# Kernel tuning notes

Hardware: AMD Instinct MI355X
Metric: run time of the kernel (lower is better)

Reference implementation:

```python
import jax, jax.numpy as jnp
import numpy as np

D_MODEL = 512
NUM_HEADS = 8
D_K = D_MODEL // NUM_HEADS


def _linear(x, w, b):
    # torch nn.Linear: y = x @ w.T + b, w: [out, in]
    return jnp.einsum('bsd,ed->bse', x, w) + b


def _attn_proj(x, w1, b1, w2, b2):
    return jax.nn.silu(_linear(x, w1, b1)) * _linear(x, w2, b2)


def setup_inputs() -> dict:
    key = jax.random.key(0)
    ks = jax.random.split(key, 20)
    B, S, D = 4, 8192, D_MODEL
    scale = 1.0 / np.sqrt(D)
    inp = {
        'query': jax.random.normal(ks[0], (B, S, D), jnp.float32),
        'key': jax.random.normal(ks[1], (B, S, D), jnp.float32),
        'value': jax.random.normal(ks[2], (B, S, D), jnp.float32),
    }
    names = ['q_w1', 'q_w2', 'k_w1', 'k_w2', 'v_w1', 'v_w2', 'out_w']
    for i, n in enumerate(names):
        inp[n] = jax.random.normal(ks[3 + i], (D, D), jnp.float32) * scale
    bnames = ['q_b1', 'q_b2', 'k_b1', 'k_b2', 'v_b1', 'v_b2', 'out_b']
    for i, n in enumerate(bnames):
        inp[n] = jax.random.normal(ks[10 + i], (D,), jnp.float32) * 0.01
    return inp


def reference(query, key, value,
              q_w1, q_w2, k_w1, k_w2, v_w1, v_w2, out_w,
              q_b1, q_b2, k_b1, k_b2, v_b1, v_b2, out_b):
    B = query.shape[0]
    eps = 1e-6
    # projections -> [B, H, S, d_k]
    def split_heads(x):
        return x.reshape(B, -1, NUM_HEADS, D_K).transpose(0, 2, 1, 3)
    q = split_heads(_attn_proj(query, q_w1, q_b1, q_w2, q_b2))
    k = split_heads(_attn_proj(key, k_w1, k_b1, k_w2, k_b2))
    v = split_heads(_attn_proj(value, v_w1, v_b1, v_w2, v_b2))

    phi_q = jax.nn.elu(q) + 1.0
    phi_k = jax.nn.elu(k) + 1.0
    # key_value: [B, H, d_k, d_k]
    key_value = jnp.einsum('bhsd,bhse->bhde', phi_k, v)
    key_sum = phi_k.sum(axis=-2)                       # [B, H, d_k]
    qk_sum = jnp.einsum('bhsd,bhd->bhs', phi_q, key_sum)
    numerator = jnp.einsum('bhsd,bhde->bhse', phi_q, key_value)
    attn = numerator / (qk_sum[..., None] + eps)       # [B, H, S, d_k]

    x = attn.transpose(0, 2, 1, 3).reshape(B, -1, NUM_HEADS * D_K)
    return _linear(x, out_w, out_b)
```

## Files before the change

### kernel.cpp

```cpp
#include <hip/hip_runtime.h>
#include <stdint.h>


#define DMODEL 512
#define NHEAD 8
#define BATCH 4
#define SEQ 8192
#define BSROWS (BATCH * SEQ)
#define NSPLIT 16
#define CHUNK (SEQ / NSPLIT)

typedef __attribute__((ext_vector_type(8))) short short8;
typedef __attribute__((ext_vector_type(4))) short short4v;
typedef __attribute__((ext_vector_type(4))) float f32x4;
typedef __attribute__((ext_vector_type(4))) unsigned short ushort4v;

__device__ __forceinline__ unsigned short f2bf(float f) {
  union { float f; uint32_t u; } v; v.f = f;
  uint32_t u = v.u;
  u += 0x7fffu + ((u >> 16) & 1u);
  return (unsigned short)(u >> 16);
}
__device__ __forceinline__ float bf2f(unsigned short h) {
  union { float f; uint32_t u; } v; v.u = ((uint32_t)h) << 16; return v.f;
}
__device__ __forceinline__ f32x4 zero4() {
  f32x4 z; z[0] = 0.f; z[1] = 0.f; z[2] = 0.f; z[3] = 0.f; return z;
}
__device__ __forceinline__ void gload_lds16(const unsigned short* g, unsigned short* l) {
  __builtin_amdgcn_global_load_lds((const __attribute__((address_space(1))) void*)g,
                                   (__attribute__((address_space(3))) void*)l, 16, 0, 0);
}

struct WPtrs { const float* w[7]; };

__global__ void convert_weights_kernel(WPtrs wp, unsigned short* __restrict__ wbf) {
  int gid = blockIdx.x * 256 + threadIdx.x;
  int which = gid >> 16;
  int rem = gid & 65535;
  float4 v = ((const float4*)wp.w[which])[rem];
  ushort4v o;
  o[0] = f2bf(v.x); o[1] = f2bf(v.y); o[2] = f2bf(v.z); o[3] = f2bf(v.w);
  *(ushort4v*)(wbf + (size_t)which * 262144 + (size_t)rem * 4) = o;
}

__global__ void convert_x_kernel(const float* __restrict__ q, const float* __restrict__ k,
                                 const float* __restrict__ v, unsigned short* __restrict__ xbf) {
  size_t t = (size_t)blockIdx.x * 256 + threadIdx.x;
  int which = (int)(t >> 21);
  size_t rem = t & 2097151;
  const float* src = which == 0 ? q : (which == 1 ? k : v);
  const float4* s4 = (const float4*)src + rem * 2;
  float4 a = s4[0], b = s4[1];
  short8 o;
  o[0] = (short)f2bf(a.x); o[1] = (short)f2bf(a.y);
  o[2] = (short)f2bf(a.z); o[3] = (short)f2bf(a.w);
  o[4] = (short)f2bf(b.x); o[5] = (short)f2bf(b.y);
  o[6] = (short)f2bf(b.z); o[7] = (short)f2bf(b.w);
  *(short8*)(xbf + ((size_t)which << 24) + rem * 8) = o;
}

struct ProjArgs {
  const float* b1[3];
  const float* b2[3];
  unsigned short* out[3];
};

__global__ __launch_bounds__(256, 2) void proj_kernel(ProjArgs pa,
                                                      const unsigned short* __restrict__ wbf,
                                                      const unsigned short* __restrict__ xbf) {
  const int which = blockIdx.y;
  const unsigned short* __restrict__ x = xbf + ((size_t)which << 24);
  const unsigned short* __restrict__ w1 = wbf + (size_t)which * 524288;
  const unsigned short* __restrict__ w2 = w1 + 262144;
  const float* __restrict__ b1p = pa.b1[which];
  const float* __restrict__ b2p = pa.b2[which];
  unsigned short* __restrict__ outp = pa.out[which];
  const bool PHI = (which < 2);

  const int mt = blockIdx.x >> 2, nt = blockIdx.x & 3;
  const int m0 = mt * 128, n0 = nt * 128;
  const int tid = threadIdx.x;
  const int wave = tid >> 6, lane = tid & 63;
  const int lrow = lane & 15, quad = lane >> 4;
  const int m_off = (wave & 1) * 64, n_off = (wave >> 1) * 64;

  __shared__ unsigned short sA[128 * 64];
  __shared__ unsigned short sB1[128 * 64];
  __shared__ unsigned short sB2[128 * 64];

  const int srow_l = lane >> 3;
  const int kq_l = (lane & 7) ^ srow_l;
  const int swz = lrow & 7;

  f32x4 acc1[4][4], acc2[4][4];
#pragma unroll
  for (int i = 0; i < 4; i++)
#pragma unroll
    for (int j = 0; j < 4; j++) { acc1[i][j] = zero4(); acc2[i][j] = zero4(); }

  for (int k0 = 0; k0 < 512; k0 += 64) {
    __syncthreads();
#pragma unroll
    for (int i = 0; i < 4; i++) {
      int ig = wave * 4 + i;
      size_t roff = (size_t)(ig * 8 + srow_l) * 512 + k0 + kq_l * 8;
      gload_lds16(x + (size_t)m0 * 512 + roff, sA + ig * 512);
      gload_lds16(w1 + (size_t)n0 * 512 + roff, sB1 + ig * 512);
      gload_lds16(w2 + (size_t)n0 * 512 + roff, sB2 + ig * 512);
    }
    __syncthreads();
#pragma unroll
    for (int kk = 0; kk < 64; kk += 32) {
      const int e8 = (kk >> 3) + quad;
      short8 af[4], b1f[4], b2f[4];
#pragma unroll
      for (int mi = 0; mi < 4; mi++)
        af[mi] = *(const short8*)(sA + (m_off + mi * 16 + lrow) * 64 + (((e8 ^ swz) << 3)));
#pragma unroll
      for (int ni = 0; ni < 4; ni++) {
        int rr = n_off + ni * 16 + lrow;
        b1f[ni] = *(const short8*)(sB1 + rr * 64 + (((e8 ^ swz) << 3)));
        b2f[ni] = *(const short8*)(sB2 + rr * 64 + (((e8 ^ swz) << 3)));
      }
#pragma unroll
      for (int ni = 0; ni < 4; ni++)
#pragma unroll
        for (int mi = 0; mi < 4; mi++) {
          acc1[mi][ni] = __builtin_amdgcn_mfma_f32_16x16x32_bf16(af[mi], b1f[ni], acc1[mi][ni], 0, 0, 0);
          acc2[mi][ni] = __builtin_amdgcn_mfma_f32_16x16x32_bf16(af[mi], b2f[ni], acc2[mi][ni], 0, 0, 0);
        }
    }
  }

  if (which == 0) {
#pragma unroll
    for (int ni = 0; ni < 4; ni++) {
      int n = n0 + n_off + ni * 16 + lrow;
      float bb1 = b1p[n], bb2 = b2p[n];
#pragma unroll
      for (int mi = 0; mi < 4; mi++)
#pragma unroll
        for (int r = 0; r < 4; r++) {
          int m = m0 + m_off + mi * 16 + quad * 4 + r;
          float v1 = acc1[mi][ni][r] + bb1;
          float v2 = acc2[mi][ni][r] + bb2;
          float y = v1 * (1.f / (1.f + __expf(-v1))) * v2;
          y = (y > 0.f) ? (y + 1.f) : __expf(y);
          outp[(size_t)m * 512 + n] = f2bf(y);
        }
    }
  } else {
    const int bI = m0 >> 13;
    const int sb = (m0 & 8191) + m_off + quad * 4;
#pragma unroll
    for (int ni = 0; ni < 4; ni++) {
      int n = n0 + n_off + ni * 16 + lrow;
      float bb1 = b1p[n], bb2 = b2p[n];
      int h = n >> 6, d = n & 63;
      unsigned short* dst0 = outp + (((size_t)bI * 8 + h) * 64 + d) * 8192 + sb;
#pragma unroll
      for (int mi = 0; mi < 4; mi++) {
        short4v o;
#pragma unroll
        for (int r = 0; r < 4; r++) {
          float v1 = acc1[mi][ni][r] + bb1;
          float v2 = acc2[mi][ni][r] + bb2;
          float y = v1 * (1.f / (1.f + __expf(-v1))) * v2;
          if (PHI) y = (y > 0.f) ? (y + 1.f) : __expf(y);
          o[r] = (short)f2bf(y);
        }
        *(short4v*)(dst0 + mi * 16) = o;
      }
    }
  }
}

__global__ __launch_bounds__(256) void kv_kernel(const unsigned short* __restrict__ kT,
                                                 const unsigned short* __restrict__ vT,
                                                 float* __restrict__ kvt_part,
                                                 float* __restrict__ ksum_part) {
  const int chunk = blockIdx.x & (NSPLIT - 1);
  const int bh = blockIdx.x >> 4;
  const int tid = threadIdx.x;
  const int wave = tid >> 6, lane = tid & 63;
  const int lrow = lane & 15, quad = lane >> 4;

  __shared__ float ls_acc[4096];
  __shared__ float ls_ksum[64];
  if (tid < 64) ls_ksum[tid] = 0.f;
#pragma unroll
  for (int i = 0; i < 16; i++) ls_acc[tid + 256 * i] = 0.f;

  const unsigned short* vrow = vT + (size_t)bh * 64 * 8192;
  const unsigned short* krow = kT + (size_t)bh * 64 * 8192;
  const int s_w = chunk * CHUNK + wave * 128;

  short8 ones;
#pragma unroll
  for (int j = 0; j < 8; j++) ones[j] = (short)0x3F80;

  f32x4 acc[4][4], aks[4];
#pragma unroll
  for (int i = 0; i < 4; i++) {
    aks[i] = zero4();
#pragma unroll
    for (int j = 0; j < 4; j++) acc[i][j] = zero4();
  }

  for (int it = 0; it < 4; it++) {
    const int s0 = s_w + it * 32 + quad * 8;
    short8 af[4], bfr[4];
#pragma unroll
    for (int mi = 0; mi < 4; mi++)
      af[mi] = *(const short8*)(vrow + (size_t)(mi * 16 + lrow) * 8192 + s0);
#pragma unroll
    for (int ni = 0; ni < 4; ni++)
      bfr[ni] = *(const short8*)(krow + (size_t)(ni * 16 + lrow) * 8192 + s0);
#pragma unroll
    for (int ni = 0; ni < 4; ni++) {
      aks[ni] = __builtin_amdgcn_mfma_f32_16x16x32_bf16(ones, bfr[ni], aks[ni], 0, 0, 0);
#pragma unroll
      for (int mi = 0; mi < 4; mi++)
        acc[mi][ni] = __builtin_amdgcn_mfma_f32_16x16x32_bf16(af[mi], bfr[ni], acc[mi][ni], 0, 0, 0);
    }
  }

  __syncthreads();
#pragma unroll
  for (int mi = 0; mi < 4; mi++)
#pragma unroll
    for (int ni = 0; ni < 4; ni++)
#pragma unroll
      for (int r = 0; r < 4; r++)
        atomicAdd(&ls_acc[(mi * 16 + quad * 4 + r) * 64 + ni * 16 + lrow], acc[mi][ni][r]);
  if (quad == 0) {
#pragma unroll
    for (int ni = 0; ni < 4; ni++) atomicAdd(&ls_ksum[ni * 16 + lrow], aks[ni][0]);
  }
  __syncthreads();

  float* op = kvt_part + ((size_t)chunk * 32 + bh) * 4096;
#pragma unroll
  for (int i = 0; i < 16; i++) op[tid + 256 * i] = ls_acc[tid + 256 * i];
  if (tid < 64) ksum_part[((size_t)chunk * 32 + bh) * 64 + tid] = ls_ksum[tid];
}

__global__ void kv_reduce_kernel(const float* __restrict__ kvt_part,
                                 const float* __restrict__ ksum_part,
                                 unsigned short* __restrict__ kvT,
                                 unsigned short* __restrict__ ksum_bf) {
  const int bh = blockIdx.x >> 2, seg = blockIdx.x & 3;
  const int idx = seg * 1024 + threadIdx.x * 4;
  float4 s = make_float4(0.f, 0.f, 0.f, 0.f);
#pragma unroll
  for (int c = 0; c < NSPLIT; c++) {
    float4 v = *(const float4*)&kvt_part[((size_t)c * 32 + bh) * 4096 + idx];
    s.x += v.x; s.y += v.y; s.z += v.z; s.w += v.w;
  }
  ushort4v o;
  o[0] = f2bf(s.x); o[1] = f2bf(s.y); o[2] = f2bf(s.z); o[3] = f2bf(s.w);
  *(ushort4v*)(kvT + (size_t)bh * 4096 + idx) = o;
  if (seg == 0 && threadIdx.x < 64) {
    float t = 0.f;
#pragma unroll
    for (int c = 0; c < NSPLIT; c++) t += ksum_part[((size_t)c * 32 + bh) * 64 + threadIdx.x];
    ksum_bf[bh * 64 + threadIdx.x] = f2bf(t);
  }
}

__global__ __launch_bounds__(256) void attn_kernel(const unsigned short* __restrict__ phiQ,
                                                   const unsigned short* __restrict__ kvT,
                                                   const unsigned short* __restrict__ ksum_bf,
                                                   unsigned short* __restrict__ xattn) {
  const int bh = blockIdx.x & 31;
  const int st = blockIdx.x >> 5;
  const int b = bh >> 3, h = bh & 7;
  const int tid = threadIdx.x;
  const int wave = tid >> 6, lane = tid & 63;
  const int lrow = lane & 15, quad = lane >> 4;
  const size_t rowbase = (size_t)b * SEQ + st * 128 + wave * 32;

  f32x4 acc[2][4], aqs[2];
#pragma unroll
  for (int i = 0; i < 2; i++) {
    aqs[i] = zero4();
#pragma unroll
    for (int j = 0; j < 4; j++) acc[i][j] = zero4();
  }

#pragma unroll
  for (int kk = 0; kk < 64; kk += 32) {
    short8 ks = *(const short8*)(ksum_bf + bh * 64 + kk + quad * 8);
    short8 af[2];
#pragma unroll
    for (int mi = 0; mi < 2; mi++)
      af[mi] = *(const short8*)(phiQ + (rowbase + mi * 16 + lrow) * 512 + h * 64 + kk + quad * 8);
#pragma unroll
    for (int mi = 0; mi < 2; mi++)
      aqs[mi] = __builtin_amdgcn_mfma_f32_16x16x32_bf16(af[mi], ks, aqs[mi], 0, 0, 0);
#pragma unroll
    for (int ni = 0; ni < 4; ni++) {
      short8 bfr = *(const short8*)(kvT + (size_t)bh * 4096 + (ni * 16 + lrow) * 64 + kk + quad * 8);
#pragma unroll
      for (int mi = 0; mi < 2; mi++)
        acc[mi][ni] = __builtin_amdgcn_mfma_f32_16x16x32_bf16(af[mi], bfr, acc[mi][ni], 0, 0, 0);
    }
  }
#pragma unroll
  for (int mi = 0; mi < 2; mi++) {
#pragma unroll
    for (int r = 0; r < 4; r++) {
      float inv = 1.f / (aqs[mi][r] + 1e-6f);
      size_t m = rowbase + mi * 16 + quad * 4 + r;
#pragma unroll
      for (int ni = 0; ni < 4; ni++)
        xattn[m * 512 + h * 64 + ni * 16 + lrow] = f2bf(acc[mi][ni][r] * inv);
    }
  }
}

__global__ __launch_bounds__(256, 2) void out_gemm_kernel(const unsigned short* __restrict__ xattn,
                                                          const unsigned short* __restrict__ wo,
                                                          const float* __restrict__ ob,
                                                          float* __restrict__ out) {
  const int mt = blockIdx.x >> 2, nt = blockIdx.x & 3;
  const int m0 = mt * 128, n0 = nt * 128;
  const int tid = threadIdx.x;
  const int wave = tid >> 6, lane = tid & 63;
  const int lrow = lane & 15, quad = lane >> 4;
  const int m_off = (wave & 1) * 64, n_off = (wave >> 1) * 64;

  __shared__ unsigned short sA[128 * 64];
  __shared__ unsigned short sB[128 * 64];

  const int srow_l = lane >> 3;
  const int kq_l = (lane & 7) ^ srow_l;
  const int swz = lrow & 7;

  f32x4 acc[4][4];
#pragma unroll
  for (int i = 0; i < 4; i++)
#pragma unroll
    for (int j = 0; j < 4; j++) acc[i][j] = zero4();

  for (int k0 = 0; k0 < 512; k0 += 64) {
    __syncthreads();
#pragma unroll
    for (int i = 0; i < 4; i++) {
      int ig = wave * 4 + i;
      size_t roff = (size_t)(ig * 8 + srow_l) * 512 + k0 + kq_l * 8;
      gload_lds16(xattn + (size_t)m0 * 512 + roff, sA + ig * 512);
      gload_lds16(wo + (size_t)n0 * 512 + roff, sB + ig * 512);
    }
    __syncthreads();
#pragma unroll
    for (int kk = 0; kk < 64; kk += 32) {
      const int e8 = (kk >> 3) + quad;
      short8 af[4], bfr[4];
#pragma unroll
      for (int mi = 0; mi < 4; mi++)
        af[mi] = *(const short8*)(sA + (m_off + mi * 16 + lrow) * 64 + (((e8 ^ swz) << 3)));
#pragma unroll
      for (int ni = 0; ni < 4; ni++)
        bfr[ni] = *(const short8*)(sB + (n_off + ni * 16 + lrow) * 64 + (((e8 ^ swz) << 3)));
#pragma unroll
      for (int ni = 0; ni < 4; ni++)
#pragma unroll
        for (int mi = 0; mi < 4; mi++)
          acc[mi][ni] = __builtin_amdgcn_mfma_f32_16x16x32_bf16(af[mi], bfr[ni], acc[mi][ni], 0, 0, 0);
    }
  }
#pragma unroll
  for (int ni = 0; ni < 4; ni++) {
    int n = n0 + n_off + ni * 16 + lrow;
    float bb = ob[n];
#pragma unroll
    for (int mi = 0; mi < 4; mi++)
#pragma unroll
      for (int r = 0; r < 4; r++) {
        int m = m0 + m_off + mi * 16 + quad * 4 + r;
        out[(size_t)m * 512 + n] = acc[mi][ni][r] + bb;
      }
  }
}

extern "C" void kernel_launch(void* const* d_in, const int* in_sizes, int n_in,
                              void* d_out, int out_size, void* d_ws, size_t ws_size,
                              hipStream_t stream) {
  char* ws = (char*)d_ws;
  size_t off = 0;
  auto alloc = [&](size_t bytes) -> void* {
    void* p = ws + off;
    off += (bytes + 255) & ~(size_t)255;
    return p;
  };
  unsigned short* wbf = (unsigned short*)alloc((size_t)7 * 262144 * 2);
  unsigned short* phiQ = (unsigned short*)alloc((size_t)BSROWS * 512 * 2);
  unsigned short* kT = (unsigned short*)alloc((size_t)BSROWS * 512 * 2);
  unsigned short* vT = (unsigned short*)alloc((size_t)BSROWS * 512 * 2);
  unsigned short* xbf = (unsigned short*)alloc((size_t)3 * BSROWS * 512 * 2);
  if (off > ws_size) return;

  char* xr = (char*)xbf;
  unsigned short* xattn = (unsigned short*)xr;
  float* kvt_part = (float*)(xr + 67108864);
  float* ksum_part = (float*)(xr + 75497472);
  unsigned short* kvT = (unsigned short*)(xr + 75628544);
  unsigned short* ksum_bf = (unsigned short*)(xr + 75890688);

  WPtrs wp;
  for (int i = 0; i < 7; i++) wp.w[i] = (const float*)d_in[3 + i];
  convert_weights_kernel<<<1792, 256, 0, stream>>>(wp, wbf);
  convert_x_kernel<<<24576, 256, 0, stream>>>((const float*)d_in[0], (const float*)d_in[1],
                                              (const float*)d_in[2], xbf);

  ProjArgs pa;
  pa.b1[0] = (const float*)d_in[10]; pa.b2[0] = (const float*)d_in[11];
  pa.b1[1] = (const float*)d_in[12]; pa.b2[1] = (const float*)d_in[13];
  pa.b1[2] = (const float*)d_in[14]; pa.b2[2] = (const float*)d_in[15];
  pa.out[0] = phiQ; pa.out[1] = kT; pa.out[2] = vT;
  proj_kernel<<<dim3(1024, 3), 256, 0, stream>>>(pa, wbf, xbf);

  kv_kernel<<<512, 256, 0, stream>>>(kT, vT, kvt_part, ksum_part);
  kv_reduce_kernel<<<128, 256, 0, stream>>>(kvt_part, ksum_part, kvT, ksum_bf);
  attn_kernel<<<2048, 256, 0, stream>>>(phiQ, kvT, ksum_bf, xattn);
  out_gemm_kernel<<<1024, 256, 0, stream>>>(xattn, wbf + (size_t)6 * 262144,
                                            (const float*)d_in[16], (float*)d_out);
}
```

Before: 476.4 us.

## Double-buffer LDS and enlarge M tile to 256 in projection and output GEMMs

Both the projection GEMM and the output GEMM now use 512-thread blocks covering a 256x128 tile, so each loaded weight tile is reused across twice as many rows. The single-buffered K loop becomes a two-stage LDS ping-pong: loads for the next K slice are issued before computing the current one, with explicit vmcnt waits and barriers. The goal is to hide global-to-LDS latency and cut redundant weight traffic. In exchange, LDS use per block rises to 128KB (proj) and 96KB (out GEMM), which may limit occupancy, and the hand-tuned vmcnt counts must match the number of loads issued.

After: 485.7 us. No clear change (+2.0%).

```diff
diff --git a/kernel.cpp b/kernel.cpp
--- a/kernel.cpp
+++ b/kernel.cpp
@@ -66,7 +66,7 @@
   unsigned short* out[3];
 };
 
-__global__ __launch_bounds__(256, 2) void proj_kernel(ProjArgs pa,
+__global__ __launch_bounds__(512, 2) void proj_kernel(ProjArgs pa,
                                                       const unsigned short* __restrict__ wbf,
                                                       const unsigned short* __restrict__ xbf) {
   const int which = blockIdx.y;
@@ -79,15 +79,13 @@
   const bool PHI = (which < 2);
 
   const int mt = blockIdx.x >> 2, nt = blockIdx.x & 3;
-  const int m0 = mt * 128, n0 = nt * 128;
+  const int m0 = mt * 256, n0 = nt * 128;
   const int tid = threadIdx.x;
   const int wave = tid >> 6, lane = tid & 63;
   const int lrow = lane & 15, quad = lane >> 4;
-  const int m_off = (wave & 1) * 64, n_off = (wave >> 1) * 64;
-
-  __shared__ unsigned short sA[128 * 64];
-  __shared__ unsigned short sB1[128 * 64];
-  __shared__ unsigned short sB2[128 * 64];
+  const int m_off = (wave >> 1) * 64, n_off = (wave & 1) * 64;
+
+  __shared__ unsigned short lds[2 * 32768];
 
   const int srow_l = lane >> 3;
   const int kq_l = (lane & 7) ^ srow_l;
@@ -99,29 +97,58 @@
 #pragma unroll
     for (int j = 0; j < 4; j++) { acc1[i][j] = zero4(); acc2[i][j] = zero4(); }
 
-  for (int k0 = 0; k0 < 512; k0 += 64) {
-    __syncthreads();
+  {
 #pragma unroll
     for (int i = 0; i < 4; i++) {
       int ig = wave * 4 + i;
-      size_t roff = (size_t)(ig * 8 + srow_l) * 512 + k0 + kq_l * 8;
-      gload_lds16(x + (size_t)m0 * 512 + roff, sA + ig * 512);
-      gload_lds16(w1 + (size_t)n0 * 512 + roff, sB1 + ig * 512);
-      gload_lds16(w2 + (size_t)n0 * 512 + roff, sB2 + ig * 512);
-    }
-    __syncthreads();
+      gload_lds16(x + (size_t)(m0 + ig * 8 + srow_l) * 512 + kq_l * 8,
+                  lds + ig * 512);
+    }
+#pragma unroll
+    for (int j = 0; j < 2; j++) {
+      int igb = wave * 2 + j;
+      size_t roff = (size_t)(n0 + igb * 8 + srow_l) * 512 + kq_l * 8;
+      gload_lds16(w1 + roff, lds + 16384 + igb * 512);
+      gload_lds16(w2 + roff, lds + 24576 + igb * 512);
+    }
+  }
+
+  for (int t = 0; t < 8; ++t) {
+    unsigned short* cur = lds + (t & 1) * 32768;
+    if (t < 7) {
+      unsigned short* nxt = lds + ((t + 1) & 1) * 32768;
+      const int k0 = (t + 1) * 64;
+#pragma unroll
+      for (int i = 0; i < 4; i++) {
+        int ig = wave * 4 + i;
+        gload_lds16(x + (size_t)(m0 + ig * 8 + srow_l) * 512 + k0 + kq_l * 8,
+                    nxt + ig * 512);
+      }
+#pragma unroll
+      for (int j = 0; j < 2; j++) {
+        int igb = wave * 2 + j;
+        size_t roff = (size_t)(n0 + igb * 8 + srow_l) * 512 + k0 + kq_l * 8;
+        gload_lds16(w1 + roff, nxt + 16384 + igb * 512);
+        gload_lds16(w2 + roff, nxt + 24576 + igb * 512);
+      }
+      asm volatile("s_waitcnt vmcnt(8)" ::: "memory");
+    } else {
+      asm volatile("s_waitcnt vmcnt(0)" ::: "memory");
+    }
+    __builtin_amdgcn_s_barrier();
+
 #pragma unroll
     for (int kk = 0; kk < 64; kk += 32) {
       const int e8 = (kk >> 3) + quad;
       short8 af[4], b1f[4], b2f[4];
 #pragma unroll
       for (int mi = 0; mi < 4; mi++)
-        af[mi] = *(const short8*)(sA + (m_off + mi * 16 + lrow) * 64 + (((e8 ^ swz) << 3)));
+        af[mi] = *(const short8*)(cur + (m_off + mi * 16 + lrow) * 64 + ((e8 ^ swz) << 3));
 #pragma unroll
       for (int ni = 0; ni < 4; ni++) {
         int rr = n_off + ni * 16 + lrow;
-        b1f[ni] = *(const short8*)(sB1 + rr * 64 + (((e8 ^ swz) << 3)));
-        b2f[ni] = *(const short8*)(sB2 + rr * 64 + (((e8 ^ swz) << 3)));
+        b1f[ni] = *(const short8*)(cur + 16384 + rr * 64 + ((e8 ^ swz) << 3));
+        b2f[ni] = *(const short8*)(cur + 24576 + rr * 64 + ((e8 ^ swz) << 3));
       }
 #pragma unroll
       for (int ni = 0; ni < 4; ni++)
@@ -131,6 +158,7 @@
           acc2[mi][ni] = __builtin_amdgcn_mfma_f32_16x16x32_bf16(af[mi], b2f[ni], acc2[mi][ni], 0, 0, 0);
         }
     }
+    __builtin_amdgcn_s_barrier();
   }
 
   if (which == 0) {
@@ -320,19 +348,18 @@
   }
 }
 
-__global__ __launch_bounds__(256, 2) void out_gemm_kernel(const unsigned short* __restrict__ xattn,
+__global__ __launch_bounds__(512, 2) void out_gemm_kernel(const unsigned short* __restrict__ xattn,
                                                           const unsigned short* __restrict__ wo,
                                                           const float* __restrict__ ob,
                                                           float* __restrict__ out) {
   const int mt = blockIdx.x >> 2, nt = blockIdx.x & 3;
-  const int m0 = mt * 128, n0 = nt * 128;
+  const int m0 = mt * 256, n0 = nt * 128;
   const int tid = threadIdx.x;
   const int wave = tid >> 6, lane = tid & 63;
   const int lrow = lane & 15, quad = lane >> 4;
-  const int m_off = (wave & 1) * 64, n_off = (wave >> 1) * 64;
-
-  __shared__ unsigned short sA[128 * 64];
-  __shared__ unsigned short sB[128 * 64];
+  const int m_off = (wave >> 1) * 64, n_off = (wave & 1) * 64;
+
+  __shared__ unsigned short lds[2 * 24576];
 
   const int srow_l = lane >> 3;
   const int kq_l = (lane & 7) ^ srow_l;
@@ -344,33 +371,63 @@
 #pragma unroll
     for (int j = 0; j < 4; j++) acc[i][j] = zero4();
 
-  for (int k0 = 0; k0 < 512; k0 += 64) {
-    __syncthreads();
+  {
 #pragma unroll
     for (int i = 0; i < 4; i++) {
       int ig = wave * 4 + i;
-      size_t roff = (size_t)(ig * 8 + srow_l) * 512 + k0 + kq_l * 8;
-      gload_lds16(xattn + (size_t)m0 * 512 + roff, sA + ig * 512);
-      gload_lds16(wo + (size_t)n0 * 512 + roff, sB + ig * 512);
-    }
-    __syncthreads();
+      gload_lds16(xattn + (size_t)(m0 + ig * 8 + srow_l) * 512 + kq_l * 8,
+                  lds + ig * 512);
+    }
+#pragma unroll
+    for (int j = 0; j < 2; j++) {
+      int igb = wave * 2 + j;
+      gload_lds16(wo + (size_t)(n0 + igb * 8 + srow_l) * 512 + kq_l * 8,
+                  lds + 16384 + igb * 512);
+    }
+  }
+
+  for (int t = 0; t < 8; ++t) {
+    unsigned short* cur = lds + (t & 1) * 24576;
+    if (t < 7) {
+      unsigned short* nxt = lds + ((t + 1) & 1) * 24576;
+      const int k0 = (t + 1) * 64;
+#pragma unroll
+      for (int i = 0; i < 4; i++) {
+        int ig = wave * 4 + i;
+        gload_lds16(xattn + (size_t)(m0 + ig * 8 + srow_l) * 512 + k0 + kq_l * 8,
+                    nxt + ig * 512);
+      }
+#pragma unroll
+      for (int j = 0; j < 2; j++) {
+        int igb = wave * 2 + j;
+        gload_lds16(wo + (size_t)(n0 + igb * 8 + srow_l) * 512 + k0 + kq_l * 8,
+                    nxt + 16384 + igb * 512);
+      }
+      asm volatile("s_waitcnt vmcnt(6)" ::: "memory");
+    } else {
+      asm volatile("s_waitcnt vmcnt(0)" ::: "memory");
+    }
+    __builtin_amdgcn_s_barrier();
+
 #pragma unroll
     for (int kk = 0; kk < 64; kk += 32) {
       const int e8 = (kk >> 3) + quad;
       short8 af[4], bfr[4];
 #pragma unroll
       for (int mi = 0; mi < 4; mi++)
-        af[mi] = *(const short8*)(sA + (m_off + mi * 16 + lrow) * 64 + (((e8 ^ swz) << 3)));
+        af[mi] = *(const short8*)(cur + (m_off + mi * 16 + lrow) * 64 + ((e8 ^ swz) << 3));
 #pragma unroll
       for (int ni = 0; ni < 4; ni++)
-        bfr[ni] = *(const short8*)(sB + (n_off + ni * 16 + lrow) * 64 + (((e8 ^ swz) << 3)));
+        bfr[ni] = *(const short8*)(cur + 16384 + (n_off + ni * 16 + lrow) * 64 + ((e8 ^ swz) << 3));
 #pragma unroll
       for (int ni = 0; ni < 4; ni++)
 #pragma unroll
         for (int mi = 0; mi < 4; mi++)
           acc[mi][ni] = __builtin_amdgcn_mfma_f32_16x16x32_bf16(af[mi], bfr[ni], acc[mi][ni], 0, 0, 0);
     }
-  }
+    __builtin_amdgcn_s_barrier();
+  }
+
 #pragma unroll
   for (int ni = 0; ni < 4; ni++) {
     int n = n0 + n_off + ni * 16 + lrow;
@@ -420,11 +477,11 @@
   pa.b1[1] = (const float*)d_in[12]; pa.b2[1] = (const float*)d_in[13];
   pa.b1[2] = (const float*)d_in[14]; pa.b2[2] = (const float*)d_in[15];
   pa.out[0] = phiQ; pa.out[1] = kT; pa.out[2] = vT;
-  proj_kernel<<<dim3(1024, 3), 256, 0, stream>>>(pa, wbf, xbf);
+  proj_kernel<<<dim3(512, 3), 512, 0, stream>>>(pa, wbf, xbf);
 
   kv_kernel<<<512, 256, 0, stream>>>(kT, vT, kvt_part, ksum_part);
   kv_reduce_kernel<<<128, 256, 0, stream>>>(kvt_part, ksum_part, kvT, ksum_bf);
   attn_kernel<<<2048, 256, 0, stream>>>(phiQ, kvT, ksum_bf, xattn);
-  out_gemm_kernel<<<1024, 256, 0, stream>>>(xattn, wbf + (size_t)6 * 262144,
-                                            (const float*)d_in[16], (float*)d_out);
-}
+  out_gemm_kernel<<<512, 512, 0, stream>>>(xattn, wbf + (size_t)6 * 262144,
+                                           (const float*)d_in[16], (float*)d_out);
+}
```
